# Optimization experiments

Hardware: AMD Instinct MI355X
Metric: run time of the kernel (lower is better)

## Reference

```python
import jax, jax.numpy as jnp
import numpy as np
import math

PATCH_SIZE = 64      # patch size at level resolution
LEVEL_RES = 512      # level resolution
TARGET_SIZE = 16     # mask patch output size
EXTRACT_SIZE = 16    # target_patch_grid_size for features
TEMPERATURE = 1.5    # temperature for entropy confidence


def _grid_sample_border(img, grid):
    """Bilinear grid_sample, padding_mode='border', align_corners=False.
    img: [C, H, W]; grid: [..., 2] (x, y) in [-1, 1]. Returns [C, ...]."""
    C, H, W = img.shape
    x = jnp.clip(((grid[..., 0] + 1.0) * W - 1.0) * 0.5, 0.0, W - 1.0)
    y = jnp.clip(((grid[..., 1] + 1.0) * H - 1.0) * 0.5, 0.0, H - 1.0)
    x0 = jnp.floor(x)
    y0 = jnp.floor(y)
    x1 = jnp.minimum(x0 + 1.0, W - 1.0)
    y1 = jnp.minimum(y0 + 1.0, H - 1.0)
    wx = x - x0
    wy = y - y0
    x0i, x1i = x0.astype(jnp.int32), x1.astype(jnp.int32)
    y0i, y1i = y0.astype(jnp.int32), y1.astype(jnp.int32)
    flat = img.reshape(C, H * W)
    gather = lambda yi, xi: jnp.take(flat, yi * W + xi, axis=1)  # [C, ...]
    v00 = gather(y0i, x0i)
    v01 = gather(y0i, x1i)
    v10 = gather(y1i, x0i)
    v11 = gather(y1i, x1i)
    top = v00 * (1.0 - wx) + v01 * wx
    bot = v10 * (1.0 - wx) + v11 * wx
    return top * (1.0 - wy) + bot * wy


def _make_grid(fh, fw, half, res, tsize):
    """fh, fw: [B, K] patch centers in pixel units at resolution `res`.
    Returns sampling grid [B, K, tsize, tsize, 2] in (x, y) normalized coords."""
    cy = fh / res * 2.0 - 1.0
    cx = fw / res * 2.0 - 1.0
    off = jnp.linspace(-half, half, tsize, dtype=jnp.float32)
    gy, gx = jnp.meshgrid(off, off, indexing='ij')
    offs = jnp.stack([gx, gy], axis=-1)             # [t, t, 2]
    centers = jnp.stack([cx, cy], axis=-1)          # [B, K, 2]
    return centers[:, :, None, None, :] + offs[None, None]


def setup_inputs() -> dict:
    key = jax.random.key(0)
    k1, k2, k3, k4 = jax.random.split(key, 4)
    B, K, D, N = 4, 32, 512, 4096
    features = jax.random.normal(k1, (B, N, D), jnp.float32)
    mask = jax.random.normal(k2, (B, 1, LEVEL_RES, LEVEL_RES), jnp.float32)
    logits = jax.random.normal(k3, (B, K, 1, 64, 64), jnp.float32)
    coords = jax.random.randint(k4, (B, K, 2), 0, LEVEL_RES - PATCH_SIZE, jnp.int32)
    return {"features": features, "mask": mask, "logits": logits, "coords": coords}


def reference(features, mask, logits, coords):
    B, N, D = features.shape
    K = coords.shape[1]
    ags = int(round(N ** 0.5))  # actual feature grid size

    # --- entropy confidence ---
    p = jnp.clip(jax.nn.sigmoid(logits / TEMPERATURE), 1e-6, 1.0 - 1e-6)
    ent = -(p * jnp.log(p) + (1.0 - p) * jnp.log(1.0 - p))
    confidence = 1.0 - ent / math.log(2.0)
    if confidence.shape[2] > 1:
        confidence = confidence.mean(axis=2, keepdims=True)

    ch = coords[..., 0].astype(jnp.float32)
    cw = coords[..., 1].astype(jnp.float32)

    # --- mask patches (grid_sample over full-res mask) ---
    grid_m = _make_grid(ch + PATCH_SIZE / 2, cw + PATCH_SIZE / 2,
                        PATCH_SIZE / LEVEL_RES, LEVEL_RES, TARGET_SIZE)
    mp = jax.vmap(_grid_sample_border)(mask, grid_m)          # [B, 1, K, t, t]
    mask_patches = jnp.transpose(mp, (0, 2, 1, 3, 4))         # [B, K, 1, t, t]

    # --- patch features (grid_sample over token feature grid) ---
    scale = ags / LEVEL_RES
    psf = max(1, int(PATCH_SIZE * scale))                     # patch size in feature px
    grid_f = _make_grid(ch * scale + psf / 2, cw * scale + psf / 2,
                        psf / ags, ags, EXTRACT_SIZE)
    feats_sp = jnp.transpose(features.reshape(B, ags, ags, D), (0, 3, 1, 2))
    pf = jax.vmap(_grid_sample_border)(feats_sp, grid_f)      # [B, D, K, E, E]
    patch_features = jnp.transpose(pf, (0, 2, 3, 4, 1)).reshape(
        B, K, EXTRACT_SIZE * EXTRACT_SIZE, D)                 # [B, K, E*E, D]

    return confidence, mask_patches, patch_features
```

## Files before the change

kernel.cpp:

```cpp
#include <hip/hip_runtime.h>
#include <math.h>

#define Bn   4
#define Kn   32
#define Dn   512
#define Nn   4096
#define AGS  64
#define RES  512
#define TS   16
#define OFF0    (-0.125f)
#define OFFSTEP (0.25f / 15.0f)

typedef float f32x4 __attribute__((ext_vector_type(4)));

#define FEAT_T (Bn * Kn * TS * TS * 64)
#define CONF_T (Bn * Kn * 64 * 64 / 4)
#define MASK_T (Bn * Kn * TS * TS)
#define TOTAL_T (FEAT_T + CONF_T + MASK_T)

__device__ __forceinline__ float unnorm_clip(float g, float size) {
    float v = ((g + 1.0f) * size - 1.0f) * 0.5f;
    return fminf(fmaxf(v, 0.0f), size - 1.0f);
}

__device__ __forceinline__ float conf_elem(float logit) {
    float s = logit * (1.0f / 1.5f);
    float e = __expf(-s);
    float p = 1.0f / (1.0f + e);
    float ent = __logf(1.0f + e) + (1.0f - p) * s;
    return 1.0f - ent * 1.4426950408889634f;
}

__global__ __launch_bounds__(256) void fused_kernel(
    const float* __restrict__ features,
    const float* __restrict__ mask,
    const float* __restrict__ logits,
    const int*   __restrict__ coords,
    float* __restrict__ out_conf,
    float* __restrict__ out_mask,
    float* __restrict__ out_feat) {

    int tid = blockIdx.x * blockDim.x + threadIdx.x;

    if (tid < FEAT_T) {
        int dc     = tid & 63;
        int sample = tid >> 6;
        int j  = sample & 15;
        int i  = (sample >> 4) & 15;
        int bk = sample >> 8;
        int b  = bk >> 5;

        float ch = (float)coords[bk * 2 + 0];
        float cw = (float)coords[bk * 2 + 1];
        float cy = (ch * 0.125f + 4.0f) * (2.0f / 64.0f) - 1.0f;
        float cx = (cw * 0.125f + 4.0f) * (2.0f / 64.0f) - 1.0f;
        float gx = cx + (OFF0 + j * OFFSTEP);
        float gy = cy + (OFF0 + i * OFFSTEP);

        float x = unnorm_clip(gx, 64.0f);
        float y = unnorm_clip(gy, 64.0f);
        float x0f = floorf(x), y0f = floorf(y);
        int x0 = (int)x0f, y0 = (int)y0f;
        int x1 = min(x0 + 1, 63), y1 = min(y0 + 1, 63);
        float wx = x - x0f, wy = y - y0f;

        const f32x4* f = (const f32x4*)(features + (size_t)b * Nn * Dn);
        int r00 = (y0 * AGS + x0) * 128 + dc;
        int r01 = (y0 * AGS + x1) * 128 + dc;
        int r10 = (y1 * AGS + x0) * 128 + dc;
        int r11 = (y1 * AGS + x1) * 128 + dc;

        f32x4 a00 = f[r00],      a01 = f[r01],      a10 = f[r10],      a11 = f[r11];
        f32x4 b00 = f[r00 + 64], b01 = f[r01 + 64], b10 = f[r10 + 64], b11 = f[r11 + 64];

        float w00 = (1.0f - wx) * (1.0f - wy);
        float w01 = wx * (1.0f - wy);
        float w10 = (1.0f - wx) * wy;
        float w11 = wx * wy;

        f32x4 ra = a00 * w00 + a01 * w01 + a10 * w10 + a11 * w11;
        f32x4 rb = b00 * w00 + b01 * w01 + b10 * w10 + b11 * w11;

        f32x4* op = (f32x4*)out_feat + (size_t)sample * 128 + dc;
        __builtin_nontemporal_store(ra, op);
        __builtin_nontemporal_store(rb, op + 64);
        return;
    }
    tid -= FEAT_T;

    if (tid < CONF_T) {
        f32x4 v = ((const f32x4*)logits)[tid];
        f32x4 r;
        r.x = conf_elem(v.x);
        r.y = conf_elem(v.y);
        r.z = conf_elem(v.z);
        r.w = conf_elem(v.w);
        __builtin_nontemporal_store(r, (f32x4*)out_conf + tid);
        return;
    }
    tid -= CONF_T;

    {
        int idx = tid;
        int j  = idx & 15;
        int i  = (idx >> 4) & 15;
        int bk = idx >> 8;
        int b  = bk >> 5;

        float ch = (float)coords[bk * 2 + 0];
        float cw = (float)coords[bk * 2 + 1];
        float cy = (ch + 32.0f) * (2.0f / 512.0f) - 1.0f;
        float cx = (cw + 32.0f) * (2.0f / 512.0f) - 1.0f;
        float gx = cx + (OFF0 + j * OFFSTEP);
        float gy = cy + (OFF0 + i * OFFSTEP);

        float x = unnorm_clip(gx, 512.0f);
        float y = unnorm_clip(gy, 512.0f);
        float x0f = floorf(x), y0f = floorf(y);
        int x0 = (int)x0f, y0 = (int)y0f;
        int x1 = min(x0 + 1, 511), y1 = min(y0 + 1, 511);
        float wx = x - x0f, wy = y - y0f;

        const float* mb = mask + (size_t)b * RES * RES;
        float v00 = mb[y0 * RES + x0];
        float v01 = mb[y0 * RES + x1];
        float v10 = mb[y1 * RES + x0];
        float v11 = mb[y1 * RES + x1];
        float top = v00 * (1.0f - wx) + v01 * wx;
        float bot = v10 * (1.0f - wx) + v11 * wx;
        float r = top * (1.0f - wy) + bot * wy;
        __builtin_nontemporal_store(r, out_mask + idx);
    }
}

extern "C" void kernel_launch(void* const* d_in, const int* in_sizes, int n_in,
                              void* d_out, int out_size, void* d_ws, size_t ws_size,
                              hipStream_t stream) {
    const float* features = (const float*)d_in[0];
    const float* mask     = (const float*)d_in[1];
    const float* logits   = (const float*)d_in[2];
    const int*   coords   = (const int*)d_in[3];

    float* out_conf = (float*)d_out;
    float* out_mask = out_conf + (size_t)Bn * Kn * 64 * 64;
    float* out_feat = out_mask + (size_t)Bn * Kn * TS * TS;

    fused_kernel<<<TOTAL_T / 256, 256, 0, stream>>>(
        features, mask, logits, coords, out_conf, out_mask, out_feat);
}
```

Measured before the change: 113.2 us.

## Stage per-patch feature window in shared memory for bilinear sampling

```diff
diff --git a/kernel.cpp b/kernel.cpp
--- a/kernel.cpp
+++ b/kernel.cpp
@@ -13,10 +13,10 @@
 
 typedef float f32x4 __attribute__((ext_vector_type(4)));
 
-#define FEAT_T (Bn * Kn * TS * TS * 64)
-#define CONF_T (Bn * Kn * 64 * 64 / 4)
-#define MASK_T (Bn * Kn * TS * TS)
-#define TOTAL_T (FEAT_T + CONF_T + MASK_T)
+#define FEAT_WGS 512
+#define CONF_WGS 512
+#define MASK_WGS 128
+#define NWG (FEAT_WGS + CONF_WGS + MASK_WGS)
 
 __device__ __forceinline__ float unnorm_clip(float g, float size) {
     float v = ((g + 1.0f) * size - 1.0f) * 0.5f;
@@ -40,55 +40,74 @@
     float* __restrict__ out_mask,
     float* __restrict__ out_feat) {
 
-    int tid = blockIdx.x * blockDim.x + threadIdx.x;
+    __shared__ f32x4 tile[100 * 32];
 
-    if (tid < FEAT_T) {
-        int dc     = tid & 63;
-        int sample = tid >> 6;
-        int j  = sample & 15;
-        int i  = (sample >> 4) & 15;
-        int bk = sample >> 8;
-        int b  = bk >> 5;
+    int wg = blockIdx.x;
+    int t  = threadIdx.x;
+
+    if (wg < FEAT_WGS) {
+        int bk     = wg >> 2;
+        int dchunk = wg & 3;
+        int b      = bk >> 5;
 
         float ch = (float)coords[bk * 2 + 0];
         float cw = (float)coords[bk * 2 + 1];
-        float cy = (ch * 0.125f + 4.0f) * (2.0f / 64.0f) - 1.0f;
-        float cx = (cw * 0.125f + 4.0f) * (2.0f / 64.0f) - 1.0f;
-        float gx = cx + (OFF0 + j * OFFSTEP);
-        float gy = cy + (OFF0 + i * OFFSTEP);
+        float fh = ch * 0.125f + 4.0f;
+        float fw = cw * 0.125f + 4.0f;
+        int r0 = min(max((int)floorf(fh - 4.5f), 0), AGS - 10);
+        int c0 = min(max((int)floorf(fw - 4.5f), 0), AGS - 10);
 
-        float x = unnorm_clip(gx, 64.0f);
-        float y = unnorm_clip(gy, 64.0f);
-        float x0f = floorf(x), y0f = floorf(y);
-        int x0 = (int)x0f, y0 = (int)y0f;
-        int x1 = min(x0 + 1, 63), y1 = min(y0 + 1, 63);
-        float wx = x - x0f, wy = y - y0f;
+        const f32x4* fsrc = (const f32x4*)(features + (size_t)b * Nn * Dn);
+        int lane = t & 31;
+        int slot = t >> 5;
+        #pragma unroll
+        for (int it = 0; it < 13; ++it) {
+            int px = it * 8 + slot;
+            if (px < 100) {
+                int r = px / 10;
+                int c = px - r * 10;
+                tile[px * 32 + lane] =
+                    fsrc[(size_t)((r0 + r) * AGS + (c0 + c)) * 128 + dchunk * 32 + lane];
+            }
+        }
+        __syncthreads();
 
-        const f32x4* f = (const f32x4*)(features + (size_t)b * Nn * Dn);
-        int r00 = (y0 * AGS + x0) * 128 + dc;
-        int r01 = (y0 * AGS + x1) * 128 + dc;
-        int r10 = (y1 * AGS + x0) * 128 + dc;
-        int r11 = (y1 * AGS + x1) * 128 + dc;
+        float cyn = fh * (2.0f / 64.0f) - 1.0f;
+        float cxn = fw * (2.0f / 64.0f) - 1.0f;
+        f32x4* outp = (f32x4*)out_feat + (size_t)bk * 256 * 128 + dchunk * 32 + lane;
 
-        f32x4 a00 = f[r00],      a01 = f[r01],      a10 = f[r10],      a11 = f[r11];
-        f32x4 b00 = f[r00 + 64], b01 = f[r01 + 64], b10 = f[r10 + 64], b11 = f[r11 + 64];
+        for (int s = 0; s < 32; ++s) {
+            int sl = slot + (s << 3);
+            int i = sl >> 4, j = sl & 15;
+            float gx = cxn + (OFF0 + j * OFFSTEP);
+            float gy = cyn + (OFF0 + i * OFFSTEP);
+            float x = unnorm_clip(gx, 64.0f);
+            float y = unnorm_clip(gy, 64.0f);
+            float x0f = floorf(x), y0f = floorf(y);
+            int x0 = (int)x0f, y0 = (int)y0f;
+            int x1 = min(x0 + 1, 63), y1 = min(y0 + 1, 63);
+            float wx = x - x0f, wy = y - y0f;
+            int xi0 = x0 - c0, xi1 = x1 - c0;
+            int yi0 = y0 - r0, yi1 = y1 - r0;
 
-        float w00 = (1.0f - wx) * (1.0f - wy);
-        float w01 = wx * (1.0f - wy);
-        float w10 = (1.0f - wx) * wy;
-        float w11 = wx * wy;
+            f32x4 v00 = tile[(yi0 * 10 + xi0) * 32 + lane];
+            f32x4 v01 = tile[(yi0 * 10 + xi1) * 32 + lane];
+            f32x4 v10 = tile[(yi1 * 10 + xi0) * 32 + lane];
+            f32x4 v11 = tile[(yi1 * 10 + xi1) * 32 + lane];
 
-        f32x4 ra = a00 * w00 + a01 * w01 + a10 * w10 + a11 * w11;
-        f32x4 rb = b00 * w00 + b01 * w01 + b10 * w10 + b11 * w11;
+            float w00 = (1.0f - wx) * (1.0f - wy);
+            float w01 = wx * (1.0f - wy);
+            float w10 = (1.0f - wx) * wy;
+            float w11 = wx * wy;
+            f32x4 res = v00 * w00 + v01 * w01 + v10 * w10 + v11 * w11;
 
-        f32x4* op = (f32x4*)out_feat + (size_t)sample * 128 + dc;
-        __builtin_nontemporal_store(ra, op);
-        __builtin_nontemporal_store(rb, op + 64);
+            __builtin_nontemporal_store(res, outp + (size_t)sl * 128);
+        }
         return;
     }
-    tid -= FEAT_T;
 
-    if (tid < CONF_T) {
+    if (wg < FEAT_WGS + CONF_WGS) {
+        int tid = (wg - FEAT_WGS) * 256 + t;
         f32x4 v = ((const f32x4*)logits)[tid];
         f32x4 r;
         r.x = conf_elem(v.x);
@@ -98,14 +117,13 @@
         __builtin_nontemporal_store(r, (f32x4*)out_conf + tid);
         return;
     }
-    tid -= CONF_T;
 
     {
-        int idx = tid;
+        int idx = (wg - FEAT_WGS - CONF_WGS) * 256 + t;
         int j  = idx & 15;
         int i  = (idx >> 4) & 15;
         int bk = idx >> 8;
-        int b  = bk >> 5;
+        int bb = bk >> 5;
 
         float ch = (float)coords[bk * 2 + 0];
         float cw = (float)coords[bk * 2 + 1];
@@ -121,7 +139,7 @@
         int x1 = min(x0 + 1, 511), y1 = min(y0 + 1, 511);
         float wx = x - x0f, wy = y - y0f;
 
-        const float* mb = mask + (size_t)b * RES * RES;
+        const float* mb = mask + (size_t)bb * RES * RES;
         float v00 = mb[y0 * RES + x0];
         float v01 = mb[y0 * RES + x1];
         float v10 = mb[y1 * RES + x0];
@@ -145,6 +163,6 @@
     float* out_mask = out_conf + (size_t)Bn * Kn * 64 * 64;
     float* out_feat = out_mask + (size_t)Bn * Kn * TS * TS;
 
-    fused_kernel<<<TOTAL_T / 256, 256, 0, stream>>>(
+    fused_kernel<<<NWG, 256, 0, stream>>>(
         features, mask, logits, coords, out_conf, out_mask, out_feat);
 }
```

Result: faster. 105.2 us (-7.1%).
